# Kernel optimization log

Hardware: AMD Instinct MI355X
Metric: run time of the kernel (lower is better)

The kernel has to match this reference:

```python
import jax, jax.numpy as jnp
import numpy as np

N, E, D_IN, H, C, D_OUT = 50000, 800000, 16, 4, 64, 32


def setup_inputs() -> dict:
    key = jax.random.key(0)
    ks = jax.random.split(key, 24)
    w = lambda k, shape: (jax.random.normal(k, shape, jnp.float32) * 0.1)
    p = {}
    p["x"] = jax.random.normal(ks[0], (N, D_IN), jnp.float32)
    p["edge_index"] = jax.random.randint(ks[1], (2, E), 0, N, jnp.int32)
    p["W1"] = w(ks[2], (D_IN, H * C))
    p["a1_src"] = w(ks[3], (H, C))
    p["a1_dst"] = w(ks[4], (H, C))
    p["b1"] = jnp.zeros((H * C,), jnp.float32)
    p["W2"] = w(ks[5], (H * C, H * C))
    p["a2_src"] = w(ks[6], (H, C))
    p["a2_dst"] = w(ks[7], (H, C))
    p["b2"] = jnp.zeros((H * C,), jnp.float32)
    # GATConv 3: 256 -> 32, 1 head, concat=False (mean)
    p["W3"] = w(ks[8], (H * C, 1 * D_OUT))
    p["a3_src"] = w(ks[9], (1, D_OUT))
    p["a3_dst"] = w(ks[10], (1, D_OUT))
    p["b3"] = jnp.zeros((D_OUT,), jnp.float32)
    # LayerNorms over 256
    p["g1"] = jnp.ones((H * C,), jnp.float32)
    p["beta1"] = jnp.zeros((H * C,), jnp.float32)
    p["g2"] = jnp.ones((H * C,), jnp.float32)
    p["beta2"] = jnp.zeros((H * C,), jnp.float32)
    # risk head: Linear(32,32) -> ReLU -> Linear(32,6) -> Sigmoid
    p["Wr1"] = w(ks[11], (D_OUT, 32))
    p["br1"] = jnp.zeros((32,), jnp.float32)
    p["Wr2"] = w(ks[12], (32, 6))
    p["br2"] = jnp.zeros((6,), jnp.float32)
    return p


def layernorm(x, g, b, eps=1e-5):
    mu = jnp.mean(x, axis=-1, keepdims=True)
    var = jnp.mean(jnp.square(x - mu), axis=-1, keepdims=True)
    return (x - mu) * jax.lax.rsqrt(var + eps) * g + b


def gat_layer(x, src, dst, W, b, a_src, a_dst, n_nodes, concat):
    # PyG GATConv (eval mode): lin -> per-edge leaky_relu score -> segment softmax over dst -> scatter sum
    heads, ch = a_src.shape
    h = (x @ W).reshape(n_nodes, heads, ch)                 # [N,H,C]
    alpha_s = jnp.sum(h * a_src[None], axis=-1)             # [N,H]
    alpha_d = jnp.sum(h * a_dst[None], axis=-1)             # [N,H]
    e = jax.nn.leaky_relu(alpha_s[src] + alpha_d[dst], 0.2)  # [E,H]
    m = jax.ops.segment_max(e, dst, num_segments=n_nodes)   # stable softmax per dst
    ex = jnp.exp(e - m[dst])
    denom = jax.ops.segment_sum(ex, dst, num_segments=n_nodes)
    alpha = ex / (denom[dst] + 1e-16)                        # [E,H]
    out = jax.ops.segment_sum(alpha[:, :, None] * h[src], dst, num_segments=n_nodes)  # [N,H,C]
    out = out.reshape(n_nodes, heads * ch) if concat else out.mean(axis=1)
    return out + b


def reference(x, edge_index, W1, a1_src, a1_dst, b1, W2, a2_src, a2_dst, b2,
              W3, a3_src, a3_dst, b3, g1, beta1, g2, beta2, Wr1, br1, Wr2, br2):
    n = x.shape[0]
    loops = jnp.arange(n, dtype=edge_index.dtype)
    src = jnp.concatenate([edge_index[0], loops])  # GATConv adds self-loops by default
    dst = jnp.concatenate([edge_index[1], loops])
    h = gat_layer(x, src, dst, W1, b1, a1_src, a1_dst, n, True)
    h = jax.nn.elu(layernorm(h, g1, beta1))
    h = gat_layer(h, src, dst, W2, b2, a2_src, a2_dst, n, True)
    h = jax.nn.elu(layernorm(h, g2, beta2))
    h = gat_layer(h, src, dst, W3, b3, a3_src, a3_dst, n, False)
    risk = jax.nn.sigmoid(jax.nn.relu(h @ Wr1 + br1) @ Wr2 + br2)
    return (h, risk)
```

## Files before the change

kernel.cpp:

```cpp
#include <hip/hip_runtime.h>
#include <hip/hip_bf16.h>
#include <cmath>

constexpr int Nn  = 50000;
constexpr int Np  = 50176;
constexpr int Ee  = 800000;
constexpr int ET  = Ee + Nn;
constexpr int F   = 256;
constexpr int DO  = 32;

constexpr int A1S=4096, A1D=4352, B1O=4608,
              A2S=4864, A2D=5120, B2O=5376,
              A3S=5632, A3D=5664, B3O=5696,
              G1O=5728, BE1O=5984, G2O=6240, BE2O=6496,
              WR1O=6752, BR1O=7776, WR2O=7808, BR2O=8000, WTOT=8006;

struct InPtrs { const void* p[22]; };

typedef __attribute__((ext_vector_type(8))) short short8v;
typedef __attribute__((ext_vector_type(8))) unsigned short ushort8v;
typedef __attribute__((ext_vector_type(4))) float f32x4;

__device__ __forceinline__ float ld_in(const void* p, int i, int bf){
  if (bf){ unsigned u = (unsigned)((const unsigned short*)p)[i];
           union{unsigned u; float f;} c; c.u = u<<16; return c.f; }
  return ((const float*)p)[i];
}
__device__ __forceinline__ float b2f(unsigned short u){
  union{unsigned u; float f;} c; c.u = ((unsigned)u)<<16; return c.f;
}
__device__ __forceinline__ unsigned short f2b(float f){
  union{float f; unsigned u;} c; c.f=f; unsigned u=c.u;
  return (unsigned short)((u + 0x7fffu + ((u>>16)&1u))>>16);
}
__device__ __forceinline__ void st_out(void* o, int bf, long i, float v){
  if (bf) ((unsigned short*)o)[i] = f2b(v);
  else ((float*)o)[i]=v;
}
__device__ __forceinline__ float wsum64(float v){
  #pragma unroll
  for (int o=32;o;o>>=1) v += __shfl_xor(v,o);
  return v;
}

__global__ void k_detect(const unsigned* __restrict__ xr, int* __restrict__ flag){
  __shared__ int cnt;
  if (threadIdx.x==0) cnt=0;
  __syncthreads();
  int bad=0;
  for (int i=threadIdx.x;i<2048;i+=256){
    unsigned lo = xr[i]&0xffffu;
    unsigned ex = (lo>>7)&0xffu;
    if (ex>=133u) bad++;
  }
  atomicAdd(&cnt,bad);
  __syncthreads();
  if (threadIdx.x==0) *flag = (cnt<8) ? 1 : 0;
}

__global__ void k_prep(InPtrs ip, float* __restrict__ wf,
                       unsigned short* __restrict__ xp,
                       unsigned short* __restrict__ w1t,
                       unsigned short* __restrict__ w2t,
                       unsigned short* __restrict__ w3t,
                       unsigned short* __restrict__ wa1t,
                       unsigned short* __restrict__ wa2t,
                       const int* __restrict__ flagp){
  int g = blockIdx.x*256 + threadIdx.x;
  int bf = *flagp;
  if (g < Np*32){
    int row=g>>5, k=g&31;
    float v = (row<Nn && k<16)? ld_in(ip.p[0], row*16+k, bf) : 0.f;
    xp[g]=f2b(v); return;
  }
  g -= Np*32;
  if (g < 256*256){
    int n=g>>8, k=g&255;
    w2t[n*256+k] = f2b(ld_in(ip.p[6], k*256+n, bf)); return;
  }
  g -= 256*256;
  if (g < 256*32){
    int n=g>>5, k=g&31;
    w1t[g] = (k<16)? f2b(ld_in(ip.p[2], k*256+n, bf)) : (unsigned short)0; return;
  }
  g -= 256*32;
  if (g < 32*256){
    int n=g>>8, k=g&255;
    w3t[n*256+k] = f2b(ld_in(ip.p[10], k*32+n, bf)); return;
  }
  g -= 32*256;
  if (g < 16*256){
    int col=g>>8, k=g&255;
    float v=0.f;
    if (col<8){
      int h=col&3;
      const void* av = (col<4)? ip.p[7] : ip.p[8];
      for (int c=0;c<64;c++)
        v += ld_in(ip.p[6], k*256 + h*64 + c, bf) * ld_in(av, h*64+c, bf);
    }
    wa2t[col*256+k] = f2b(v); return;
  }
  g -= 16*256;
  if (g < 16*32){
    int col=g>>5, k=g&31;
    float v=0.f;
    if (col<8 && k<16){
      int h=col&3;
      const void* av = (col<4)? ip.p[3] : ip.p[4];
      for (int c=0;c<64;c++)
        v += ld_in(ip.p[2], k*256 + h*64 + c, bf) * ld_in(av, h*64+c, bf);
    }
    wa1t[col*32+k] = f2b(v); return;
  }
  g -= 16*32;
  const int SIX[17]={3,4,5,7,8,9,11,12,13,14,15,16,17,18,19,20,21};
  const int SOF[17]={A1S,A1D,B1O,A2S,A2D,B2O,A3S,A3D,B3O,
                     G1O,BE1O,G2O,BE2O,WR1O,BR1O,WR2O,BR2O};
  const int SSZ[17]={256,256,256,256,256,256,32,32,32,
                     256,256,256,256,1024,32,192,6};
  for (int j=0;j<17;j++){
    if (g < SSZ[j]){ wf[SOF[j]+g] = ld_in(ip.p[SIX[j]], g, bf); return; }
    g -= SSZ[j];
  }
}

__global__ void k_count(const int* __restrict__ ei, int* __restrict__ deg){
  int g = blockIdx.x*256 + threadIdx.x;
  if (g < Ee) atomicAdd(&deg[ei[Ee+g]], 1);
}
__global__ void __launch_bounds__(256) k_scan_blk(const int* __restrict__ deg,
                                                  int* __restrict__ offtmp,
                                                  int* __restrict__ bsum){
  __shared__ int s[256];
  int t = threadIdx.x, i = blockIdx.x*256 + t;
  int v = (i<Nn) ? deg[i]+1 : 0;
  s[t]=v; __syncthreads();
  #pragma unroll
  for (int d=1; d<256; d<<=1){
    int x = (t>=d)? s[t-d] : 0; __syncthreads();
    s[t]+=x; __syncthreads();
  }
  if (i<Nn) offtmp[i] = s[t]-v;
  if (t==255) bsum[blockIdx.x] = s[255];
}
__global__ void __launch_bounds__(256) k_scan_top(const int* __restrict__ bsum,
                                                  int* __restrict__ bpre,
                                                  int* __restrict__ off){
  __shared__ int s[256];
  int t=threadIdx.x;
  int v = (t<196)? bsum[t]:0;
  s[t]=v; __syncthreads();
  #pragma unroll
  for (int d=1;d<256;d<<=1){ int x=(t>=d)?s[t-d]:0; __syncthreads(); s[t]+=x; __syncthreads(); }
  if (t<196) bpre[t]=s[t]-v;
  if (t==0) off[Nn]=ET;
}
__global__ void __launch_bounds__(256) k_scan_add(const int* __restrict__ offtmp,
                                                  const int* __restrict__ bpre,
                                                  int* __restrict__ off,
                                                  int* __restrict__ cursor){
  int i = blockIdx.x*256 + threadIdx.x;
  if (i<Nn){ int st = offtmp[i]+bpre[i>>8]; off[i]=st; cursor[i]=st; }
}
__global__ void k_fill(const int* __restrict__ ei, int* __restrict__ cursor,
                       int* __restrict__ csr){
  int g = blockIdx.x*256 + threadIdx.x;
  if (g < Ee){
    int s = ei[g], d = ei[Ee+g];
    int p = atomicAdd(&cursor[d],1);
    csr[p] = s;
  } else if (g < ET){
    int n = g - Ee;
    int p = atomicAdd(&cursor[n],1);
    csr[p] = n;
  }
}

template<int BM,int BN,int WAVES_M,int WAVES_N,int KT,int EPI>
__device__ __forceinline__ void gemm_body(int bid,
                                          const unsigned short* __restrict__ Ag,
                                          const unsigned short* __restrict__ BTg,
                                          unsigned short* __restrict__ Cg,
                                          const float* __restrict__ aswp,
                                          const float* __restrict__ adwp,
                                          float* __restrict__ aso,
                                          float* __restrict__ ado,
                                          int M, int N, int nMB,
                                          unsigned short* As, unsigned short* Bs){
  constexpr int WMT = BM/(WAVES_M*16);
  constexpr int WNT = BN/(WAVES_N*16);
  int bm = bid % nMB, bn = bid / nMB;
  int row0 = bm*BM, col0 = bn*BN;
  int tid = threadIdx.x, lane = tid&63, wid = tid>>6;
  int wm = wid % WAVES_M, wn = wid / WAVES_M;
  f32x4 acc[WMT][WNT];
  #pragma unroll
  for (int m=0;m<WMT;m++)
    #pragma unroll
    for (int n=0;n<WNT;n++){ acc[m][n].x=0.f; acc[m][n].y=0.f; acc[m][n].z=0.f; acc[m][n].w=0.f; }

  int cl = lane>>4, rl = lane&15;
  for (int kk=0; kk<KT; kk+=32){
    __syncthreads();
    for (int idx=tid; idx<4*BM; idx+=256){
      int r = idx>>2, c = idx&3;
      short8v v = *(const short8v*)(Ag + (size_t)(row0+r)*KT + kk + c*8);
      *(short8v*)(As + (c*BM + (r ^ (c<<2)))*8) = v;
    }
    for (int idx=tid; idx<4*BN; idx+=256){
      int r = idx>>2, c = idx&3;
      short8v v = *(const short8v*)(BTg + (size_t)(col0+r)*KT + kk + c*8);
      *(short8v*)(Bs + (c*BN + (r ^ (c<<2)))*8) = v;
    }
    __syncthreads();
    short8v af[WMT], bfv[WNT];
    #pragma unroll
    for (int m=0;m<WMT;m++){
      int r = wm*WMT*16 + m*16 + rl;
      af[m] = *(const short8v*)(As + (cl*BM + (r ^ (cl<<2)))*8);
    }
    #pragma unroll
    for (int n=0;n<WNT;n++){
      int r = wn*WNT*16 + n*16 + rl;
      bfv[n] = *(const short8v*)(Bs + (cl*BN + (r ^ (cl<<2)))*8);
    }
    #pragma unroll
    for (int m=0;m<WMT;m++)
      #pragma unroll
      for (int n=0;n<WNT;n++)
        acc[m][n] = __builtin_amdgcn_mfma_f32_16x16x32_bf16(af[m], bfv[n], acc[m][n], 0,0,0);
  }
  if constexpr (EPI==3){
    #pragma unroll
    for (int m=0;m<WMT;m++){
      int rbase = row0 + wm*WMT*16 + m*16 + (lane>>4)*4;
      int col = lane&15;
      #pragma unroll
      for (int q=0;q<4;q++){
        int row = rbase + q;
        if (row < M){
          if (col < 4)      aso[(size_t)row*4 + col]     = acc[m][0][q];
          else if (col < 8) ado[(size_t)row*4 + col - 4] = acc[m][0][q];
        }
      }
    }
    return;
  }
  #pragma unroll
  for (int m=0;m<WMT;m++){
    int rbase = row0 + wm*WMT*16 + m*16 + (lane>>4)*4;
    #pragma unroll
    for (int n=0;n<WNT;n++){
      int col = col0 + wn*WNT*16 + n*16 + (lane&15);
      #pragma unroll
      for (int q=0;q<4;q++){
        int row = rbase + q;
        if (row < M) Cg[(size_t)row*N + col] = f2b(acc[m][n][q]);
      }
    }
  }
  if constexpr (EPI==2){
    #pragma unroll
    for (int m=0;m<WMT;m++){
      #pragma unroll
      for (int q=0;q<4;q++){
        float ps=0,pd=0;
        #pragma unroll
        for (int n=0;n<WNT;n++){
          int col = n*16 + (lane&15);
          float av = acc[m][n][q];
          ps += av*aswp[col]; pd += av*adwp[col];
        }
        #pragma unroll
        for (int o=1;o<16;o<<=1){ ps+=__shfl_xor(ps,o); pd+=__shfl_xor(pd,o); }
        int row = row0 + wm*(WMT*16) + m*16 + (lane>>4)*4 + q;
        if ((lane&15)==0 && row<M){ aso[row]=ps; ado[row]=pd; }
      }
    }
  }
}

template<int KT>
__global__ void __launch_bounds__(256) k_gemm_plus(const unsigned short* __restrict__ Ag,
                                                   const unsigned short* __restrict__ BTw,
                                                   const unsigned short* __restrict__ BTa,
                                                   unsigned short* __restrict__ Cg,
                                                   float* __restrict__ as4o,
                                                   float* __restrict__ ad4o,
                                                   int M, int nMB){
  __shared__ unsigned short As[4096];
  __shared__ unsigned short Bs[4096];
  int bid = blockIdx.x;
  if (bid < nMB*2)
    gemm_body<128,128,2,2,KT,0>(bid, Ag, BTw, Cg, nullptr,nullptr,nullptr,nullptr,
                                M, 256, nMB, As, Bs);
  else
    gemm_body<128,16,4,1,KT,3>(bid - nMB*2, Ag, BTa, nullptr, nullptr,nullptr,
                               as4o, ad4o, M, 16, nMB, As, Bs);
}

__global__ void __launch_bounds__(256) k_gemm3(const unsigned short* __restrict__ Ag,
                                               const unsigned short* __restrict__ BTg,
                                               unsigned short* __restrict__ Cg,
                                               const float* __restrict__ aswp,
                                               const float* __restrict__ adwp,
                                               float* __restrict__ s3,
                                               float* __restrict__ d3,
                                               int M, int nMB){
  __shared__ unsigned short As[4096];
  __shared__ unsigned short Bs[4096];
  gemm_body<128,32,4,1,256,2>(blockIdx.x, Ag, BTg, Cg, aswp, adwp, s3, d3,
                              M, 32, nMB, As, Bs);
}

__global__ void __launch_bounds__(256) k_agg(const unsigned short* __restrict__ Hs,
                                             const float* __restrict__ as4,
                                             const float* __restrict__ ad4,
                                             const float* __restrict__ bias,
                                             const float* __restrict__ gam,
                                             const float* __restrict__ bet,
                                             const int* __restrict__ off,
                                             const int* __restrict__ csr,
                                             unsigned short* __restrict__ out){
  __shared__ float wl[4][256];
  __shared__ int   sl[4][64];
  int tid = threadIdx.x, wid = tid>>6, lane = tid&63;
  int n = blockIdx.x*4 + wid;
  if (n>=Nn) return;
  float* wlw = wl[wid];
  int*   slw = sl[wid];
  const float4 adv = *reinterpret_cast<const float4*>(ad4 + (size_t)n*4);
  int half = lane>>5, c8 = lane&31, h = c8>>3;
  const unsigned short* hbase = Hs + c8*8;
  int o0=off[n], o1=off[n+1];
  float a0=0,a1=0,a2=0,a3=0,a4=0,a5=0,a6=0,a7=0,den=0;
  for (int cb=o0; cb<o1; cb+=64){
    int m = o1-cb; if (m>64) m=64;
    if (lane < m){
      int s = csr[cb+lane];
      slw[lane] = s;
      const float4 av = *reinterpret_cast<const float4*>(as4 + (size_t)s*4);
      float t0=av.x+adv.x; t0=t0>0.f?t0:0.2f*t0;
      float t1=av.y+adv.y; t1=t1>0.f?t1:0.2f*t1;
      float t2=av.z+adv.z; t2=t2>0.f?t2:0.2f*t2;
      float t3=av.w+adv.w; t3=t3>0.f?t3:0.2f*t3;
      float4 wv; wv.x=__expf(t0); wv.y=__expf(t1); wv.z=__expf(t2); wv.w=__expf(t3);
      *reinterpret_cast<float4*>(wlw + lane*4) = wv;
    }
    int mh = m>>1;
    int lo = half? mh : 0;
    int hi = half? m  : mh;
    int i = lo;
    for (; i+3<hi; i+=4){
      int s0=slw[i], s1=slw[i+1], s2=slw[i+2], s3v=slw[i+3];
      float w0=wlw[i*4+h], w1=wlw[(i+1)*4+h], w2=wlw[(i+2)*4+h], w3=wlw[(i+3)*4+h];
      const ushort8v hv0 = *reinterpret_cast<const ushort8v*>(hbase + (size_t)s0*F);
      const ushort8v hv1 = *reinterpret_cast<const ushort8v*>(hbase + (size_t)s1*F);
      const ushort8v hv2 = *reinterpret_cast<const ushort8v*>(hbase + (size_t)s2*F);
      const ushort8v hv3 = *reinterpret_cast<const ushort8v*>(hbase + (size_t)s3v*F);
      den += (w0+w1)+(w2+w3);
      a0 += w0*b2f(hv0[0]) + w1*b2f(hv1[0]) + w2*b2f(hv2[0]) + w3*b2f(hv3[0]);
      a1 += w0*b2f(hv0[1]) + w1*b2f(hv1[1]) + w2*b2f(hv2[1]) + w3*b2f(hv3[1]);
      a2 += w0*b2f(hv0[2]) + w1*b2f(hv1[2]) + w2*b2f(hv2[2]) + w3*b2f(hv3[2]);
      a3 += w0*b2f(hv0[3]) + w1*b2f(hv1[3]) + w2*b2f(hv2[3]) + w3*b2f(hv3[3]);
      a4 += w0*b2f(hv0[4]) + w1*b2f(hv1[4]) + w2*b2f(hv2[4]) + w3*b2f(hv3[4]);
      a5 += w0*b2f(hv0[5]) + w1*b2f(hv1[5]) + w2*b2f(hv2[5]) + w3*b2f(hv3[5]);
      a6 += w0*b2f(hv0[6]) + w1*b2f(hv1[6]) + w2*b2f(hv2[6]) + w3*b2f(hv3[6]);
      a7 += w0*b2f(hv0[7]) + w1*b2f(hv1[7]) + w2*b2f(hv2[7]) + w3*b2f(hv3[7]);
    }
    for (; i<hi; ++i){
      int sv=slw[i];
      float w=wlw[i*4+h];
      const ushort8v hv = *reinterpret_cast<const ushort8v*>(hbase + (size_t)sv*F);
      den += w;
      a0 += w*b2f(hv[0]); a1 += w*b2f(hv[1]); a2 += w*b2f(hv[2]); a3 += w*b2f(hv[3]);
      a4 += w*b2f(hv[4]); a5 += w*b2f(hv[5]); a6 += w*b2f(hv[6]); a7 += w*b2f(hv[7]);
    }
  }
  a0 += __shfl_xor(a0,32); a1 += __shfl_xor(a1,32);
  a2 += __shfl_xor(a2,32); a3 += __shfl_xor(a3,32);
  a4 += __shfl_xor(a4,32); a5 += __shfl_xor(a5,32);
  a6 += __shfl_xor(a6,32); a7 += __shfl_xor(a7,32);
  den += __shfl_xor(den,32);
  float rs = 1.f/(den + 1e-16f);
  int c = c8*8;
  const float4 bv0 = *reinterpret_cast<const float4*>(bias + c);
  const float4 bv1 = *reinterpret_cast<const float4*>(bias + c + 4);
  a0=a0*rs+bv0.x; a1=a1*rs+bv0.y; a2=a2*rs+bv0.z; a3=a3*rs+bv0.w;
  a4=a4*rs+bv1.x; a5=a5*rs+bv1.y; a6=a6*rs+bv1.z; a7=a7*rs+bv1.w;
  float sl2 = a0+a1+a2+a3+a4+a5+a6+a7;
  float mu = wsum64(sl2)*(1.f/512.f);
  float d0=a0-mu,d1=a1-mu,d2=a2-mu,d3=a3-mu,d4=a4-mu,d5=a5-mu,d6=a6-mu,d7=a7-mu;
  float ql = d0*d0+d1*d1+d2*d2+d3*d3+d4*d4+d5*d5+d6*d6+d7*d7;
  float var = wsum64(ql)*(1.f/512.f);
  float r = rsqrtf(var + 1e-5f);
  const float4 gv0 = *reinterpret_cast<const float4*>(gam + c);
  const float4 gv1 = *reinterpret_cast<const float4*>(gam + c + 4);
  const float4 ev0 = *reinterpret_cast<const float4*>(bet + c);
  const float4 ev1 = *reinterpret_cast<const float4*>(bet + c + 4);
  float y0=d0*r*gv0.x+ev0.x, y1=d1*r*gv0.y+ev0.y, y2=d2*r*gv0.z+ev0.z, y3=d3*r*gv0.w+ev0.w;
  float y4=d4*r*gv1.x+ev1.x, y5=d5*r*gv1.y+ev1.y, y6=d6*r*gv1.z+ev1.z, y7=d7*r*gv1.w+ev1.w;
  y0=y0>0.f?y0:expm1f(y0); y1=y1>0.f?y1:expm1f(y1);
  y2=y2>0.f?y2:expm1f(y2); y3=y3>0.f?y3:expm1f(y3);
  y4=y4>0.f?y4:expm1f(y4); y5=y5>0.f?y5:expm1f(y5);
  y6=y6>0.f?y6:expm1f(y6); y7=y7>0.f?y7:expm1f(y7);
  if (half==0){
    ushort8v ov;
    ov[0]=f2b(y0); ov[1]=f2b(y1); ov[2]=f2b(y2); ov[3]=f2b(y3);
    ov[4]=f2b(y4); ov[5]=f2b(y5); ov[6]=f2b(y6); ov[7]=f2b(y7);
    *reinterpret_cast<ushort8v*>(out + (size_t)n*F + c) = ov;
  }
}

__global__ void __launch_bounds__(256) k_agg3r(const unsigned short* __restrict__ C3,
                                               const float* __restrict__ s3,
                                               const float* __restrict__ d3,
                                               const float* __restrict__ wf,
                                               const int* __restrict__ off,
                                               const int* __restrict__ csr,
                                               void* __restrict__ dout,
                                               const int* __restrict__ flagp){
  __shared__ float w3l[4][64];
  __shared__ int   s3l[4][64];
  int tid=threadIdx.x, wid=tid>>6, lane=tid&63;
  int n = blockIdx.x*4 + wid;
  if (n>=Nn) return;
  int bf = *flagp;
  float* wlw = w3l[wid];
  int*   slw = s3l[wid];
  int g = lane>>3, j = lane&7;
  float dn = d3[n];
  int o0=off[n], o1=off[n+1];
  float a0=0,a1=0,a2=0,a3=0,den=0;
  for (int cb=o0; cb<o1; cb+=64){
    int m = o1-cb; if (m>64) m=64;
    if (lane<m){
      int s = csr[cb+lane];
      slw[lane]=s;
      float t = s3[s] + dn; t = t>0.f? t : 0.2f*t;
      wlw[lane] = __expf(t);
    }
    for (int i=g; i<m; i+=8){
      int s=slw[i];
      float w=wlw[i];
      const ushort4 hv = *reinterpret_cast<const ushort4*>(C3 + (size_t)s*DO + j*4);
      den += w;
      a0 += w*b2f(hv.x); a1 += w*b2f(hv.y); a2 += w*b2f(hv.z); a3 += w*b2f(hv.w);
    }
  }
  #pragma unroll
  for (int o=8;o<64;o<<=1){
    a0 += __shfl_xor(a0,o); a1 += __shfl_xor(a1,o);
    a2 += __shfl_xor(a2,o); a3 += __shfl_xor(a3,o);
    den += __shfl_xor(den,o);
  }
  float rs = 1.f/(den + 1e-16f);
  const float4 bv = *reinterpret_cast<const float4*>(wf + B3O + j*4);
  float v0=a0*rs+bv.x, v1=a1*rs+bv.y, v2=a2*rs+bv.z, v3=a3*rs+bv.w;
  if (lane<8){
    long bo = (long)n*DO + lane*4;
    st_out(dout,bf,bo  ,v0); st_out(dout,bf,bo+1,v1);
    st_out(dout,bf,bo+2,v2); st_out(dout,bf,bo+3,v3);
  }
  float hk[32];
  #pragma unroll
  for (int k=0;k<32;k++){
    float src = ((k&3)==0)? v0 : ((k&3)==1)? v1 : ((k&3)==2)? v2 : v3;
    hk[k] = __shfl(src, k>>2);
  }
  float t1 = 0.f;
  if (lane<32){
    t1 = wf[BR1O+lane];
    #pragma unroll
    for (int k=0;k<32;k++) t1 += hk[k]*wf[WR1O + k*32 + lane];
    t1 = fmaxf(t1, 0.f);
  }
  float p0=0,p1=0,p2=0,p3=0,p4=0,p5=0;
  if (lane<32){
    const float* w2r = wf + WR2O + lane*6;
    p0=t1*w2r[0]; p1=t1*w2r[1]; p2=t1*w2r[2];
    p3=t1*w2r[3]; p4=t1*w2r[4]; p5=t1*w2r[5];
  }
  #pragma unroll
  for (int m=1;m<64;m<<=1){
    p0+=__shfl_xor(p0,m); p1+=__shfl_xor(p1,m); p2+=__shfl_xor(p2,m);
    p3+=__shfl_xor(p3,m); p4+=__shfl_xor(p4,m); p5+=__shfl_xor(p5,m);
  }
  if (lane<6){
    float s = (lane==0)?p0:(lane==1)?p1:(lane==2)?p2:(lane==3)?p3:(lane==4)?p4:p5;
    s += wf[BR2O+lane];
    float r = 1.f/(1.f+__expf(-s));
    st_out(dout, bf, (long)Nn*32 + (long)n*6 + lane, r);
  }
}

extern "C" void kernel_launch(void* const* d_in, const int* in_sizes, int n_in,
                              void* d_out, int out_size, void* d_ws, size_t ws_size,
                              hipStream_t stream){
  char* base = (char*)d_ws;
  size_t cur = 0;
  auto alloc = [&](size_t bytes)->char*{
    cur = (cur + 255) & ~(size_t)255;
    char* r = base + cur; cur += bytes; return r;
  };
  int*   flag = (int*)  alloc(4);
  float* wf   = (float*)alloc(sizeof(float)*WTOT);
  unsigned short* xpad = (unsigned short*)alloc(sizeof(short)*(size_t)Np*32);
  unsigned short* w1t  = (unsigned short*)alloc(sizeof(short)*256*32);
  unsigned short* w2t  = (unsigned short*)alloc(sizeof(short)*256*256);
  unsigned short* w3t  = (unsigned short*)alloc(sizeof(short)*32*256);
  unsigned short* wa1t = (unsigned short*)alloc(sizeof(short)*16*32);
  unsigned short* wa2t = (unsigned short*)alloc(sizeof(short)*16*256);
  int*   deg  = (int*)  alloc(sizeof(int)*Nn);
  int*   offt = (int*)  alloc(sizeof(int)*Nn);
  int*   bsum = (int*)  alloc(sizeof(int)*256);
  int*   bpre = (int*)  alloc(sizeof(int)*256);
  int*   off  = (int*)  alloc(sizeof(int)*(Nn+1));
  int*   curs = (int*)  alloc(sizeof(int)*Nn);
  int*   csr  = (int*)  alloc(sizeof(int)*ET);
  unsigned short* G  = (unsigned short*)alloc(sizeof(short)*(size_t)Np*F);
  unsigned short* Hb = (unsigned short*)alloc(sizeof(short)*(size_t)Np*F);
  unsigned short* C3 = (unsigned short*)alloc(sizeof(short)*(size_t)Np*DO);
  float* as4  = (float*)alloc(sizeof(float)*(size_t)Np*4);
  float* ad4  = (float*)alloc(sizeof(float)*(size_t)Np*4);
  float* s3   = (float*)alloc(sizeof(float)*Nn);
  float* d3   = (float*)alloc(sizeof(float)*Nn);

  const int* ei = (const int*)d_in[1];
  InPtrs ip;
  for (int i=0;i<22;i++) ip.p[i]=d_in[i];

  k_detect<<<1,256,0,stream>>>((const unsigned*)d_in[0], flag);
  {
    int total = Np*32 + 256*256 + 256*32 + 32*256 + 16*256 + 16*32 + 3910;
    k_prep<<<(total+255)/256,256,0,stream>>>(ip, wf, xpad, w1t, w2t, w3t, wa1t, wa2t, flag);
  }
  (void)hipMemsetAsync(deg, 0, sizeof(int)*Nn, stream);
  k_count<<<(Ee+255)/256,256,0,stream>>>(ei, deg);
  k_scan_blk<<<196,256,0,stream>>>(deg, offt, bsum);
  k_scan_top<<<1,256,0,stream>>>(bsum, bpre, off);
  k_scan_add<<<196,256,0,stream>>>(offt, bpre, off, curs);
  k_fill<<<(ET+255)/256,256,0,stream>>>(ei, curs, csr);

  dim3 wg((Nn+3)/4);
  constexpr int NMB = (Nn+127)/128;
  k_gemm_plus<32><<<NMB*3,256,0,stream>>>(xpad, w1t, wa1t, G, as4, ad4, Nn, NMB);
  k_agg<<<wg,256,0,stream>>>(G, as4, ad4, wf+B1O, wf+G1O, wf+BE1O, off, csr, Hb);
  k_gemm_plus<256><<<NMB*3,256,0,stream>>>(Hb, w2t, wa2t, G, as4, ad4, Nn, NMB);
  k_agg<<<wg,256,0,stream>>>(G, as4, ad4, wf+B2O, wf+G2O, wf+BE2O, off, csr, Hb);
  k_gemm3<<<NMB,256,0,stream>>>(Hb, w3t, C3, wf+A3S, wf+A3D, s3, d3, Nn, NMB);
  k_agg3r<<<wg,256,0,stream>>>(C3, s3, d3, wf, off, csr, d_out, flag);
}
```

Measured before the change: 445.7 us.

## Use direct global-to-LDS loads in GEMM, merge scan kernels, fold memset into prep

The GEMM tile staging now uses global_load_lds, which writes global data straight into LDS. The XOR swizzle is dropped in favour of a column-major cell layout, and a plain-copy path remains as a fallback. The degree memset moves into the prep kernel, and the two-stage top-scan plus add is merged into one kernel, which removes launches. The aggregation inner loops now unpack bf16 pairs into packed f32x2 FMAs. Removing the swizzle may bring back LDS bank conflicts on the fragment reads.

```diff
diff --git a/kernel.cpp b/kernel.cpp
--- a/kernel.cpp
+++ b/kernel.cpp
@@ -18,8 +18,25 @@
 struct InPtrs { const void* p[22]; };
 
 typedef __attribute__((ext_vector_type(8))) short short8v;
-typedef __attribute__((ext_vector_type(8))) unsigned short ushort8v;
+typedef __attribute__((ext_vector_type(2))) float f32x2;
 typedef __attribute__((ext_vector_type(4))) float f32x4;
+
+#if defined(__has_builtin)
+#if __has_builtin(__builtin_amdgcn_global_load_lds)
+#define HAS_GLD_LDS 1
+#endif
+#endif
+#ifndef HAS_GLD_LDS
+#define HAS_GLD_LDS 0
+#endif
+
+__device__ __forceinline__ void gld_lds16(const unsigned short* gp, unsigned short* lp){
+#if HAS_GLD_LDS
+  __builtin_amdgcn_global_load_lds(
+      (const __attribute__((address_space(1))) void*)gp,
+      (__attribute__((address_space(3))) void*)lp, 16, 0, 0);
+#endif
+}
 
 __device__ __forceinline__ float ld_in(const void* p, int i, int bf){
   if (bf){ unsigned u = (unsigned)((const unsigned short*)p)[i];
@@ -41,6 +58,11 @@
   #pragma unroll
   for (int o=32;o;o>>=1) v += __shfl_xor(v,o);
   return v;
+}
+__device__ __forceinline__ f32x2 up2(unsigned u){
+  union{unsigned q; float f;} a, b;
+  a.q = u<<16; b.q = u & 0xffff0000u;
+  f32x2 r; r.x=a.f; r.y=b.f; return r;
 }
 
 __global__ void k_detect(const unsigned* __restrict__ xr, int* __restrict__ flag){
@@ -65,9 +87,12 @@
                        unsigned short* __restrict__ w3t,
                        unsigned short* __restrict__ wa1t,
                        unsigned short* __restrict__ wa2t,
+                       int* __restrict__ deg,
                        const int* __restrict__ flagp){
   int g = blockIdx.x*256 + threadIdx.x;
   int bf = *flagp;
+  if (g < Nn){ deg[g] = 0; return; }
+  g -= Nn;
   if (g < Np*32){
     int row=g>>5, k=g&31;
     float v = (row<Nn && k<16)? ld_in(ip.p[0], row*16+k, bf) : 0.f;
@@ -143,24 +168,23 @@
   if (i<Nn) offtmp[i] = s[t]-v;
   if (t==255) bsum[blockIdx.x] = s[255];
 }
-__global__ void __launch_bounds__(256) k_scan_top(const int* __restrict__ bsum,
-                                                  int* __restrict__ bpre,
-                                                  int* __restrict__ off){
+__global__ void __launch_bounds__(256) k_scan_add2(const int* __restrict__ offtmp,
+                                                   const int* __restrict__ bsum,
+                                                   int* __restrict__ off,
+                                                   int* __restrict__ cursor){
   __shared__ int s[256];
-  int t=threadIdx.x;
-  int v = (t<196)? bsum[t]:0;
+  int t = threadIdx.x;
+  int v = (t<196)? bsum[t] : 0;
   s[t]=v; __syncthreads();
   #pragma unroll
-  for (int d=1;d<256;d<<=1){ int x=(t>=d)?s[t-d]:0; __syncthreads(); s[t]+=x; __syncthreads(); }
-  if (t<196) bpre[t]=s[t]-v;
-  if (t==0) off[Nn]=ET;
-}
-__global__ void __launch_bounds__(256) k_scan_add(const int* __restrict__ offtmp,
-                                                  const int* __restrict__ bpre,
-                                                  int* __restrict__ off,
-                                                  int* __restrict__ cursor){
-  int i = blockIdx.x*256 + threadIdx.x;
-  if (i<Nn){ int st = offtmp[i]+bpre[i>>8]; off[i]=st; cursor[i]=st; }
+  for (int d=1; d<256; d<<=1){
+    int x=(t>=d)?s[t-d]:0; __syncthreads();
+    s[t]+=x; __syncthreads();
+  }
+  int bpre = s[blockIdx.x] - bsum[blockIdx.x];
+  int i = blockIdx.x*256 + t;
+  if (i<Nn){ int st = offtmp[i]+bpre; off[i]=st; cursor[i]=st; }
+  if (blockIdx.x==0 && t==0) off[Nn]=ET;
 }
 __global__ void k_fill(const int* __restrict__ ei, int* __restrict__ cursor,
                        int* __restrict__ csr){
@@ -187,6 +211,7 @@
                                           float* __restrict__ ado,
                                           int M, int N, int nMB,
                                           unsigned short* As, unsigned short* Bs){
+  static_assert(BM==128, "staging assumes BM=128");
   constexpr int WMT = BM/(WAVES_M*16);
   constexpr int WNT = BN/(WAVES_N*16);
   int bm = bid % nMB, bn = bid / nMB;
@@ -202,27 +227,38 @@
   int cl = lane>>4, rl = lane&15;
   for (int kk=0; kk<KT; kk+=32){
     __syncthreads();
+#if HAS_GLD_LDS
+    for (int cb = wid*64; cb < 4*BM; cb += 256){
+      int cell = cb + lane;
+      int c = cell / BM, r = cell % BM;
+      gld_lds16(Ag + (size_t)(row0+r)*KT + kk + c*8, As + (size_t)cb*8);
+    }
+    for (int cb = wid*64; cb < 4*BN; cb += 256){
+      int cell = cb + lane;
+      int c = cell / BN, r = cell % BN;
+      gld_lds16(BTg + (size_t)(col0+r)*KT + kk + c*8, Bs + (size_t)cb*8);
+    }
+#else
     for (int idx=tid; idx<4*BM; idx+=256){
-      int r = idx>>2, c = idx&3;
-      short8v v = *(const short8v*)(Ag + (size_t)(row0+r)*KT + kk + c*8);
-      *(short8v*)(As + (c*BM + (r ^ (c<<2)))*8) = v;
+      int c = idx / BM, r = idx % BM;
+      *(short8v*)(As + (size_t)idx*8) = *(const short8v*)(Ag + (size_t)(row0+r)*KT + kk + c*8);
     }
     for (int idx=tid; idx<4*BN; idx+=256){
-      int r = idx>>2, c = idx&3;
-      short8v v = *(const short8v*)(BTg + (size_t)(col0+r)*KT + kk + c*8);
-      *(short8v*)(Bs + (c*BN + (r ^ (c<<2)))*8) = v;
-    }
+      int c = idx / BN, r = idx % BN;
+      *(short8v*)(Bs + (size_t)idx*8) = *(const short8v*)(BTg + (size_t)(col0+r)*KT + kk + c*8);
+    }
+#endif
     __syncthreads();
     short8v af[WMT], bfv[WNT];
     #pragma unroll
     for (int m=0;m<WMT;m++){
-      int r = wm*WMT*16 + m*16 + rl;
-      af[m] = *(const short8v*)(As + (cl*BM + (r ^ (cl<<2)))*8);
+      int r = wm*(WMT*16) + m*16 + rl;
+      af[m] = *(const short8v*)(As + (size_t)(cl*BM + r)*8);
     }
     #pragma unroll
     for (int n=0;n<WNT;n++){
-      int r = wn*WNT*16 + n*16 + rl;
-      bfv[n] = *(const short8v*)(Bs + (cl*BN + (r ^ (cl<<2)))*8);
+      int r = wn*(WNT*16) + n*16 + rl;
+      bfv[n] = *(const short8v*)(Bs + (size_t)(cl*BN + r)*8);
     }
     #pragma unroll
     for (int m=0;m<WMT;m++)
@@ -233,7 +269,7 @@
   if constexpr (EPI==3){
     #pragma unroll
     for (int m=0;m<WMT;m++){
-      int rbase = row0 + wm*WMT*16 + m*16 + (lane>>4)*4;
+      int rbase = row0 + wm*(WMT*16) + m*16 + (lane>>4)*4;
       int col = lane&15;
       #pragma unroll
       for (int q=0;q<4;q++){
@@ -248,10 +284,10 @@
   }
   #pragma unroll
   for (int m=0;m<WMT;m++){
-    int rbase = row0 + wm*WMT*16 + m*16 + (lane>>4)*4;
+    int rbase = row0 + wm*(WMT*16) + m*16 + (lane>>4)*4;
     #pragma unroll
     for (int n=0;n<WNT;n++){
-      int col = col0 + wn*WNT*16 + n*16 + (lane&15);
+      int col = col0 + wn*(WNT*16) + n*16 + (lane&15);
       #pragma unroll
       for (int q=0;q<4;q++){
         int row = rbase + q;
@@ -288,8 +324,8 @@
                                                    float* __restrict__ as4o,
                                                    float* __restrict__ ad4o,
                                                    int M, int nMB){
-  __shared__ unsigned short As[4096];
-  __shared__ unsigned short Bs[4096];
+  __shared__ alignas(16) unsigned short As[4096];
+  __shared__ alignas(16) unsigned short Bs[4096];
   int bid = blockIdx.x;
   if (bid < nMB*2)
     gemm_body<128,128,2,2,KT,0>(bid, Ag, BTw, Cg, nullptr,nullptr,nullptr,nullptr,
@@ -307,8 +343,8 @@
                                                float* __restrict__ s3,
                                                float* __restrict__ d3,
                                                int M, int nMB){
-  __shared__ unsigned short As[4096];
-  __shared__ unsigned short Bs[4096];
+  __shared__ alignas(16) unsigned short As[4096];
+  __shared__ alignas(16) unsigned short Bs[4096];
   gemm_body<128,32,4,1,256,2>(blockIdx.x, Ag, BTg, Cg, aswp, adwp, s3, d3,
                               M, 32, nMB, As, Bs);
 }
@@ -322,8 +358,8 @@
                                              const int* __restrict__ off,
                                              const int* __restrict__ csr,
                                              unsigned short* __restrict__ out){
-  __shared__ float wl[4][256];
-  __shared__ int   sl[4][64];
+  __shared__ alignas(16) float wl[4][256];
+  __shared__ int sl[4][64];
   int tid = threadIdx.x, wid = tid>>6, lane = tid&63;
   int n = blockIdx.x*4 + wid;
   if (n>=Nn) return;
@@ -333,7 +369,8 @@
   int half = lane>>5, c8 = lane&31, h = c8>>3;
   const unsigned short* hbase = Hs + c8*8;
   int o0=off[n], o1=off[n+1];
-  float a0=0,a1=0,a2=0,a3=0,a4=0,a5=0,a6=0,a7=0,den=0;
+  f32x2 c0={0.f,0.f}, c1={0.f,0.f}, c2={0.f,0.f}, c3={0.f,0.f};
+  float den=0.f;
   for (int cb=o0; cb<o1; cb+=64){
     int m = o1-cb; if (m>64) m=64;
     if (lane < m){
@@ -354,29 +391,27 @@
     for (; i+3<hi; i+=4){
       int s0=slw[i], s1=slw[i+1], s2=slw[i+2], s3v=slw[i+3];
       float w0=wlw[i*4+h], w1=wlw[(i+1)*4+h], w2=wlw[(i+2)*4+h], w3=wlw[(i+3)*4+h];
-      const ushort8v hv0 = *reinterpret_cast<const ushort8v*>(hbase + (size_t)s0*F);
-      const ushort8v hv1 = *reinterpret_cast<const ushort8v*>(hbase + (size_t)s1*F);
-      const ushort8v hv2 = *reinterpret_cast<const ushort8v*>(hbase + (size_t)s2*F);
-      const ushort8v hv3 = *reinterpret_cast<const ushort8v*>(hbase + (size_t)s3v*F);
+      const uint4 q0 = *reinterpret_cast<const uint4*>(hbase + (size_t)s0*F);
+      const uint4 q1 = *reinterpret_cast<const uint4*>(hbase + (size_t)s1*F);
+      const uint4 q2 = *reinterpret_cast<const uint4*>(hbase + (size_t)s2*F);
+      const uint4 q3 = *reinterpret_cast<const uint4*>(hbase + (size_t)s3v*F);
       den += (w0+w1)+(w2+w3);
-      a0 += w0*b2f(hv0[0]) + w1*b2f(hv1[0]) + w2*b2f(hv2[0]) + w3*b2f(hv3[0]);
-      a1 += w0*b2f(hv0[1]) + w1*b2f(hv1[1]) + w2*b2f(hv2[1]) + w3*b2f(hv3[1]);
-      a2 += w0*b2f(hv0[2]) + w1*b2f(hv1[2]) + w2*b2f(hv2[2]) + w3*b2f(hv3[2]);
-      a3 += w0*b2f(hv0[3]) + w1*b2f(hv1[3]) + w2*b2f(hv2[3]) + w3*b2f(hv3[3]);
-      a4 += w0*b2f(hv0[4]) + w1*b2f(hv1[4]) + w2*b2f(hv2[4]) + w3*b2f(hv3[4]);
-      a5 += w0*b2f(hv0[5]) + w1*b2f(hv1[5]) + w2*b2f(hv2[5]) + w3*b2f(hv3[5]);
-      a6 += w0*b2f(hv0[6]) + w1*b2f(hv1[6]) + w2*b2f(hv2[6]) + w3*b2f(hv3[6]);
-      a7 += w0*b2f(hv0[7]) + w1*b2f(hv1[7]) + w2*b2f(hv2[7]) + w3*b2f(hv3[7]);
+      f32x2 W0={w0,w0}, W1={w1,w1}, W2={w2,w2}, W3={w3,w3};
+      c0 += W0*up2(q0.x) + W1*up2(q1.x) + W2*up2(q2.x) + W3*up2(q3.x);
+      c1 += W0*up2(q0.y) + W1*up2(q1.y) + W2*up2(q2.y) + W3*up2(q3.y);
+      c2 += W0*up2(q0.z) + W1*up2(q1.z) + W2*up2(q2.z) + W3*up2(q3.z);
+      c3 += W0*up2(q0.w) + W1*up2(q1.w) + W2*up2(q2.w) + W3*up2(q3.w);
     }
     for (; i<hi; ++i){
       int sv=slw[i];
       float w=wlw[i*4+h];
-      const ushort8v hv = *reinterpret_cast<const ushort8v*>(hbase + (size_t)sv*F);
+      const uint4 q = *reinterpret_cast<const uint4*>(hbase + (size_t)sv*F);
       den += w;
-      a0 += w*b2f(hv[0]); a1 += w*b2f(hv[1]); a2 += w*b2f(hv[2]); a3 += w*b2f(hv[3]);
-      a4 += w*b2f(hv[4]); a5 += w*b2f(hv[5]); a6 += w*b2f(hv[6]); a7 += w*b2f(hv[7]);
-    }
-  }
+      f32x2 W={w,w};
+      c0 += W*up2(q.x); c1 += W*up2(q.y); c2 += W*up2(q.z); c3 += W*up2(q.w);
+    }
+  }
+  float a0=c0.x, a1=c0.y, a2=c1.x, a3=c1.y, a4=c2.x, a5=c2.y, a6=c3.x, a7=c3.y;
   a0 += __shfl_xor(a0,32); a1 += __shfl_xor(a1,32);
   a2 += __shfl_xor(a2,32); a3 += __shfl_xor(a3,32);
   a4 += __shfl_xor(a4,32); a5 += __shfl_xor(a5,32);
@@ -405,10 +440,10 @@
   y4=y4>0.f?y4:expm1f(y4); y5=y5>0.f?y5:expm1f(y5);
   y6=y6>0.f?y6:expm1f(y6); y7=y7>0.f?y7:expm1f(y7);
   if (half==0){
-    ushort8v ov;
-    ov[0]=f2b(y0); ov[1]=f2b(y1); ov[2]=f2b(y2); ov[3]=f2b(y3);
-    ov[4]=f2b(y4); ov[5]=f2b(y5); ov[6]=f2b(y6); ov[7]=f2b(y7);
-    *reinterpret_cast<ushort8v*>(out + (size_t)n*F + c) = ov;
+    short8v ov;
+    ov[0]=(short)f2b(y0); ov[1]=(short)f2b(y1); ov[2]=(short)f2b(y2); ov[3]=(short)f2b(y3);
+    ov[4]=(short)f2b(y4); ov[5]=(short)f2b(y5); ov[6]=(short)f2b(y6); ov[7]=(short)f2b(y7);
+    *reinterpret_cast<short8v*>(out + (size_t)n*F + c) = ov;
   }
 }
 
@@ -431,7 +466,8 @@
   int g = lane>>3, j = lane&7;
   float dn = d3[n];
   int o0=off[n], o1=off[n+1];
-  float a0=0,a1=0,a2=0,a3=0,den=0;
+  f32x2 c01={0.f,0.f}, c23={0.f,0.f};
+  float den=0.f;
   for (int cb=o0; cb<o1; cb+=64){
     int m = o1-cb; if (m>64) m=64;
     if (lane<m){
@@ -443,11 +479,13 @@
     for (int i=g; i<m; i+=8){
       int s=slw[i];
       float w=wlw[i];
-      const ushort4 hv = *reinterpret_cast<const ushort4*>(C3 + (size_t)s*DO + j*4);
+      const uint2 q = *reinterpret_cast<const uint2*>(C3 + (size_t)s*DO + j*4);
       den += w;
-      a0 += w*b2f(hv.x); a1 += w*b2f(hv.y); a2 += w*b2f(hv.z); a3 += w*b2f(hv.w);
-    }
-  }
+      f32x2 W={w,w};
+      c01 += W*up2(q.x); c23 += W*up2(q.y);
+    }
+  }
+  float a0=c01.x, a1=c01.y, a2=c23.x, a3=c23.y;
   #pragma unroll
   for (int o=8;o<64;o<<=1){
     a0 += __shfl_xor(a0,o); a1 += __shfl_xor(a1,o);
@@ -482,9 +520,9 @@
     p3=t1*w2r[3]; p4=t1*w2r[4]; p5=t1*w2r[5];
   }
   #pragma unroll
-  for (int m=1;m<64;m<<=1){
-    p0+=__shfl_xor(p0,m); p1+=__shfl_xor(p1,m); p2+=__shfl_xor(p2,m);
-    p3+=__shfl_xor(p3,m); p4+=__shfl_xor(p4,m); p5+=__shfl_xor(p5,m);
+  for (int mm=1;mm<64;mm<<=1){
+    p0+=__shfl_xor(p0,mm); p1+=__shfl_xor(p1,mm); p2+=__shfl_xor(p2,mm);
+    p3+=__shfl_xor(p3,mm); p4+=__shfl_xor(p4,mm); p5+=__shfl_xor(p5,mm);
   }
   if (lane<6){
     float s = (lane==0)?p0:(lane==1)?p1:(lane==2)?p2:(lane==3)?p3:(lane==4)?p4:p5;
@@ -514,7 +552,6 @@
   int*   deg  = (int*)  alloc(sizeof(int)*Nn);
   int*   offt = (int*)  alloc(sizeof(int)*Nn);
   int*   bsum = (int*)  alloc(sizeof(int)*256);
-  int*   bpre = (int*)  alloc(sizeof(int)*256);
   int*   off  = (int*)  alloc(sizeof(int)*(Nn+1));
   int*   curs = (int*)  alloc(sizeof(int)*Nn);
   int*   csr  = (int*)  alloc(sizeof(int)*ET);
@@ -532,14 +569,12 @@
 
   k_detect<<<1,256,0,stream>>>((const unsigned*)d_in[0], flag);
   {
-    int total = Np*32 + 256*256 + 256*32 + 32*256 + 16*256 + 16*32 + 3910;
-    k_prep<<<(total+255)/256,256,0,stream>>>(ip, wf, xpad, w1t, w2t, w3t, wa1t, wa2t, flag);
-  }
-  (void)hipMemsetAsync(deg, 0, sizeof(int)*Nn, stream);
+    int total = Nn + Np*32 + 256*256 + 256*32 + 32*256 + 16*256 + 16*32 + 3910;
+    k_prep<<<(total+255)/256,256,0,stream>>>(ip, wf, xpad, w1t, w2t, w3t, wa1t, wa2t, deg, flag);
+  }
   k_count<<<(Ee+255)/256,256,0,stream>>>(ei, deg);
   k_scan_blk<<<196,256,0,stream>>>(deg, offt, bsum);
-  k_scan_top<<<1,256,0,stream>>>(bsum, bpre, off);
-  k_scan_add<<<196,256,0,stream>>>(offt, bpre, off, curs);
+  k_scan_add2<<<196,256,0,stream>>>(offt, bsum, off, curs);
   k_fill<<<(ET+255)/256,256,0,stream>>>(ei, curs, csr);
 
   dim3 wg((Nn+3)/4);
```

Result: faster. 432.0 us (-3.1%).
